# Performance work log

Hardware: AMD Instinct MI355X
Metric: run time of the kernel (lower is better)

Reference implementation:

```python
import jax, jax.numpy as jnp
import numpy as np

H, HKV, DH = 32, 8, 128
ROPE_BASE = 500000.0


def _rope(x, pos):
    # x: [B, H, T, D]; MLX non-traditional rope (split halves)
    D = x.shape[-1]
    half = D // 2
    freqs = ROPE_BASE ** (-(jnp.arange(half, dtype=jnp.float32) * 2.0 / D))  # [half]
    t = pos + jnp.arange(x.shape[2], dtype=jnp.float32)                      # [T]
    ang = t[:, None] * freqs[None, :]                                        # [T, half]
    cos, sin = jnp.cos(ang), jnp.sin(ang)
    x1, x2 = x[..., :half], x[..., half:]
    return jnp.concatenate([x1 * cos - x2 * sin, x1 * sin + x2 * cos], axis=-1)


def setup_inputs() -> dict:
    key = jax.random.key(0)
    ks = jax.random.split(key, 5)
    B, T, HID = 1, 2048, 4096
    s = 0.02
    return {
        "hidden_states": jax.random.normal(ks[0], (B, T, HID), jnp.float32),
        "Wq": jax.random.normal(ks[1], (H * DH, HID), jnp.float32) * s,
        "Wk": jax.random.normal(ks[2], (HKV * DH, HID), jnp.float32) * s,
        "Wv": jax.random.normal(ks[3], (HKV * DH, HID), jnp.float32) * s,
        "Wo": jax.random.normal(ks[4], (HID, H * DH), jnp.float32) * s,
        "k_cache": jnp.zeros((1, HKV, 4096, DH), jnp.float32),
        "v_cache": jnp.zeros((1, HKV, 4096, DH), jnp.float32),
        "pos_int": 0,
    }


def reference(hidden_states, Wq, Wk, Wv, Wo, k_cache, v_cache, pos_int):
    B, T, _ = hidden_states.shape
    # QKV projections (no bias, Llama-style) -> [B, h, T, D]
    q = (hidden_states @ Wq.T).reshape(B, T, H, DH).transpose(0, 2, 1, 3)
    k = (hidden_states @ Wk.T).reshape(B, T, HKV, DH).transpose(0, 2, 1, 3)
    v = (hidden_states @ Wv.T).reshape(B, T, HKV, DH).transpose(0, 2, 1, 3)
    # RoPE with position offset
    q = _rope(q, pos_int)
    k = _rope(k, pos_int)
    # KV-cache scatter update at pos_int, then window to [:pos_int+T]
    k_cache = jax.lax.dynamic_update_slice(k_cache, k, (0, 0, pos_int, 0))
    v_cache = jax.lax.dynamic_update_slice(v_cache, v, (0, 0, pos_int, 0))
    Tk = pos_int + T
    k_win = k_cache[:, :, :Tk, :]
    v_win = v_cache[:, :, :Tk, :]
    # GQA: repeat_interleave KV heads to match query heads
    group = H // HKV
    k_ = jnp.repeat(k_win, group, axis=1)   # [B, H, Tk, D]
    v_ = jnp.repeat(v_win, group, axis=1)
    # SDPA, is_causal=True => top-left aligned causal mask (query i sees keys j<=i)
    scale = 1.0 / jnp.sqrt(jnp.asarray(DH, jnp.float32))
    scores = jnp.einsum("bhtd,bhsd->bhts", q, k_) * scale  # [B, H, T, Tk]
    causal = jnp.arange(Tk)[None, :] <= jnp.arange(T)[:, None]
    scores = jnp.where(causal[None, None], scores, jnp.finfo(scores.dtype).min)
    attn = jax.nn.softmax(scores, axis=-1)
    out = jnp.einsum("bhts,bhsd->bhtd", attn, v_)           # [B, H, T, D]
    out = out.transpose(0, 2, 1, 3).reshape(B, T, H * DH)
    return out @ Wo.T
```

## Files before the change

kernel.cpp:

```cpp
#include <hip/hip_runtime.h>


#define DEVI __device__ __forceinline__

typedef __attribute__((ext_vector_type(8))) short short8;
typedef __attribute__((ext_vector_type(4))) float f32x4;

DEVI unsigned short f2bf(float f) {
  union { float f; unsigned u; } x; x.f = f;
  unsigned r = x.u + 0x7FFFu + ((x.u >> 16) & 1u);
  return (unsigned short)(r >> 16);
}
DEVI float bf2f(unsigned short h) {
  union { unsigned u; float f; } x; x.u = ((unsigned)h) << 16;
  return x.f;
}
DEVI f32x4 mfma16(short8 a, short8 b, f32x4 c) {
  return __builtin_amdgcn_mfma_f32_16x16x32_bf16(a, b, c, 0, 0, 0);
}
DEVI void gl2lds16(const unsigned short* g, unsigned short* l) {
  __builtin_amdgcn_global_load_lds(
      (const __attribute__((address_space(1))) unsigned int*)g,
      (__attribute__((address_space(3))) unsigned int*)l, 16, 0, 0);
}

__global__ __launch_bounds__(256)
void cvt_kernel(const float* __restrict__ src, unsigned short* __restrict__ dst,
                int n4) {
  int i = blockIdx.x * 256 + threadIdx.x;
  const int stride = gridDim.x * 256;
  for (; i < n4; i += stride) {
    float4 v = ((const float4*)src)[i];
    ushort4 h;
    h.x = f2bf(v.x); h.y = f2bf(v.y); h.z = f2bf(v.z); h.w = f2bf(v.w);
    ((ushort4*)dst)[i] = h;
  }
}

__global__ __launch_bounds__(256, 2)
void gemm_qkv_bf16(const unsigned short* __restrict__ hsb,
                   const unsigned short* __restrict__ Wqb,
                   const unsigned short* __restrict__ Wkb,
                   const unsigned short* __restrict__ Wvb,
                   unsigned short* __restrict__ Qb,
                   unsigned short* __restrict__ Kb,
                   unsigned short* __restrict__ Vb) {
  const int K = 4096;
  __shared__ __align__(16) unsigned short As[128][64];
  __shared__ __align__(16) unsigned short Bs[128][64];
  const int tid = threadIdx.x, lane = tid & 63, wid = tid >> 6;
  const int m0 = blockIdx.y * 128;
  const int n0g = blockIdx.x * 128;

  const unsigned short* Bsrc; unsigned short* outp; int ldo, oc;
  if (n0g < 4096)      { Bsrc = Wqb + (size_t)n0g * K;          outp = Qb; ldo = 4096; oc = n0g; }
  else if (n0g < 5120) { Bsrc = Wkb + (size_t)(n0g - 4096) * K; outp = Kb; ldo = 1024; oc = n0g - 4096; }
  else                 { Bsrc = Wvb + (size_t)(n0g - 5120) * K; outp = Vb; ldo = 1024; oc = n0g - 5120; }
  const unsigned short* Asrc = hsb + (size_t)m0 * K;

  f32x4 acc[4][4];
#pragma unroll
  for (int i = 0; i < 4; ++i)
#pragma unroll
    for (int j = 0; j < 4; ++j) acc[i][j] = (f32x4){0.f, 0.f, 0.f, 0.f};

  const int wm = (wid >> 1) * 64, wn = (wid & 1) * 64;
  const int srow = wid * 32 + (lane >> 3);
  const int scol = (lane & 7) * 8;

  for (int k0 = 0; k0 < K; k0 += 64) {
#pragma unroll
    for (int i = 0; i < 4; ++i) {
      gl2lds16(Asrc + (size_t)(srow + i * 8) * K + k0 + scol, &As[wid * 32 + i * 8][0]);
      gl2lds16(Bsrc + (size_t)(srow + i * 8) * K + k0 + scol, &Bs[wid * 32 + i * 8][0]);
    }
    __syncthreads();
#pragma unroll
    for (int ks = 0; ks < 2; ++ks) {
      short8 af[4], bfr[4];
      const int co = ks * 64 + ((lane >> 4) << 4);
#pragma unroll
      for (int i = 0; i < 4; ++i) {
        af[i]  = *(const short8*)((const char*)(&As[wm + i * 16 + (lane & 15)][0]) + co);
        bfr[i] = *(const short8*)((const char*)(&Bs[wn + i * 16 + (lane & 15)][0]) + co);
      }
#pragma unroll
      for (int i = 0; i < 4; ++i)
#pragma unroll
        for (int j = 0; j < 4; ++j)
          acc[i][j] = mfma16(af[i], bfr[j], acc[i][j]);
    }
    __syncthreads();
  }

#pragma unroll
  for (int i = 0; i < 4; ++i) {
    int rb = m0 + wm + i * 16 + ((lane >> 4) << 2);
#pragma unroll
    for (int j = 0; j < 4; ++j) {
      int cb = oc + wn + j * 16 + (lane & 15);
#pragma unroll
      for (int r = 0; r < 4; ++r)
        outp[(size_t)(rb + r) * ldo + cb] = f2bf(acc[i][j][r]);
    }
  }
}

__global__ __launch_bounds__(256)
void transpose_v(const unsigned short* __restrict__ Vb,
                 unsigned short* __restrict__ VtG) {
  __shared__ unsigned short tile[64][68];
  const int tid = threadIdx.x;
  const int t0 = blockIdx.x * 64;
  const int c0 = blockIdx.y * 64;
  const int r = tid >> 4;
  const int c4 = (tid & 15) << 2;
#pragma unroll
  for (int i = 0; i < 4; ++i) {
    ushort4 v = *(const ushort4*)(Vb + (size_t)(t0 + r + i * 16) * 1024 + c0 + c4);
    *(ushort4*)&tile[r + i * 16][c4] = v;
  }
  __syncthreads();
#pragma unroll
  for (int i = 0; i < 4; ++i) {
    int d = r + i * 16;
    ushort4 o;
    o.x = tile[c4 + 0][d]; o.y = tile[c4 + 1][d];
    o.z = tile[c4 + 2][d]; o.w = tile[c4 + 3][d];
    *(ushort4*)(VtG + (size_t)(c0 + d) * 2048 + t0 + c4) = o;
  }
}

__global__ __launch_bounds__(256)
void rope_kernel(unsigned short* __restrict__ Qb, unsigned short* __restrict__ Kb,
                 const int* __restrict__ posp) {
  const int QP = 2048 * 32 * 64;
  const int KP = 2048 * 8 * 64;
  int idx = blockIdx.x * 256 + threadIdx.x;
  if (idx >= QP + KP) return;
  unsigned short* base; int t, hh, d, ld;
  if (idx < QP) {
    base = Qb; ld = 4096;
    t = idx >> 11; int rem = idx & 2047; hh = rem >> 6; d = rem & 63;
  } else {
    int j = idx - QP; base = Kb; ld = 1024;
    t = j >> 9; int rem = j & 511; hh = rem >> 6; d = rem & 63;
  }
  float freq = exp2f(-(float)d * 0.29580575880077f);
  float ang = (float)(t + posp[0]) * freq;
  float s, c;
  __sincosf(ang, &s, &c);
  size_t i1 = (size_t)t * ld + hh * 128 + d;
  float x1 = bf2f(base[i1]), x2 = bf2f(base[i1 + 64]);
  base[i1]      = f2bf(x1 * c - x2 * s);
  base[i1 + 64] = f2bf(x1 * s + x2 * c);
}

__global__ __launch_bounds__(512, 4)
void attn_kernel(const unsigned short* __restrict__ Qb,
                 const unsigned short* __restrict__ Kb,
                 const unsigned short* __restrict__ VtG,
                 unsigned short* __restrict__ Ob) {
  __shared__ __align__(16) unsigned short Ks[64][128];
  __shared__ __align__(16) unsigned short Vt[128][64];
  __shared__ __align__(16) unsigned short Ps[8][16][64];
  const int tid = threadIdx.x, lane = tid & 63, w = tid >> 6;
  const int h = blockIdx.y;
  const int qt = (blockIdx.y >> 4) ? (15 - blockIdx.x) : blockIdx.x;
  const int kh = h >> 2;
  const int q0 = qt * 128;
  const float SCALE = 0.08838834764831845f;

  short8 aq[4];
  {
    const int qrow = q0 + w * 16 + (lane & 15);
#pragma unroll
    for (int ks = 0; ks < 4; ++ks)
      aq[ks] = *(const short8*)(Qb + (size_t)qrow * 4096 + h * 128 + ks * 32 +
                                ((lane >> 4) << 3));
  }

  f32x4 o_acc[8];
#pragma unroll
  for (int n8 = 0; n8 < 8; ++n8) o_acc[n8] = (f32x4){0.f, 0.f, 0.f, 0.f};
  float mst[4], lst[4];
#pragma unroll
  for (int r = 0; r < 4; ++r) { mst[r] = -1e30f; lst[r] = 0.f; }

  const int ksrow0 = w * 8 + (lane >> 4);
  const int vdrow0 = w * 16 + (lane >> 3);

  const int ntiles = 2 * (qt + 1);
  for (int st = 0; st < ntiles; ++st) {
    const int s0 = st * 64;
#pragma unroll
    for (int j = 0; j < 2; ++j) {
      int sr = ksrow0 + j * 4;
      int sc = (((lane & 15) << 4) ^ ((sr & 7) << 4)) >> 1;
      gl2lds16(Kb + (size_t)(s0 + sr) * 1024 + kh * 128 + sc, &Ks[w * 8 + j * 4][0]);
    }
#pragma unroll
    for (int j = 0; j < 2; ++j) {
      int dr = vdrow0 + j * 8;
      int sc = (((lane & 7) << 4) ^ ((dr & 7) << 4)) >> 1;
      gl2lds16(VtG + (size_t)(kh * 128 + dr) * 2048 + s0 + sc, &Vt[w * 16 + j * 8][0]);
    }
    __syncthreads();

    f32x4 sacc[4];
#pragma unroll
    for (int ni = 0; ni < 4; ++ni) sacc[ni] = (f32x4){0.f, 0.f, 0.f, 0.f};
#pragma unroll
    for (int ks = 0; ks < 4; ++ks) {
      const int co = ks * 64 + ((lane >> 4) << 4);
      short8 bk[4];
#pragma unroll
      for (int ni = 0; ni < 4; ++ni) {
        int kr = ni * 16 + (lane & 15);
        bk[ni] = *(const short8*)((const char*)(&Ks[kr][0]) + (co ^ ((kr & 7) << 4)));
      }
#pragma unroll
      for (int ni = 0; ni < 4; ++ni)
        sacc[ni] = mfma16(aq[ks], bk[ni], sacc[ni]);
    }

    char* pb = (char*)(&Ps[w][0][0]);
#pragma unroll
    for (int r = 0; r < 4; ++r) {
      const int qrow = q0 + w * 16 + ((lane >> 4) << 2) + r;
      float v4[4]; float vmax = -1e30f;
#pragma unroll
      for (int ni = 0; ni < 4; ++ni) {
        int scol = s0 + ni * 16 + (lane & 15);
        float x = sacc[ni][r] * SCALE;
        if (scol > qrow) x = -1e30f;
        v4[ni] = x; vmax = fmaxf(vmax, x);
      }
      vmax = fmaxf(vmax, __shfl_xor(vmax, 1));
      vmax = fmaxf(vmax, __shfl_xor(vmax, 2));
      vmax = fmaxf(vmax, __shfl_xor(vmax, 4));
      vmax = fmaxf(vmax, __shfl_xor(vmax, 8));
      float mo = mst[r];
      float mn = fmaxf(mo, vmax);
      float al = __expf(mo - mn);
      float rs = 0.f;
      const int prow = ((lane >> 4) << 2) + r;
      const int pswz = ((prow >> 2) & 3) << 5;
#pragma unroll
      for (int ni = 0; ni < 4; ++ni) {
        float p = __expf(v4[ni] - mn);
        rs += p;
        int cbyte = (ni * 16 + (lane & 15)) * 2;
        *(unsigned short*)(pb + prow * 128 + (cbyte ^ pswz)) = f2bf(p);
      }
      rs += __shfl_xor(rs, 1);
      rs += __shfl_xor(rs, 2);
      rs += __shfl_xor(rs, 4);
      rs += __shfl_xor(rs, 8);
      lst[r] = lst[r] * al + rs;
      mst[r] = mn;
#pragma unroll
      for (int n8 = 0; n8 < 8; ++n8) o_acc[n8][r] *= al;
    }

#pragma unroll
    for (int ks2 = 0; ks2 < 2; ++ks2) {
      const int co = ks2 * 64 + ((lane >> 4) << 4);
      const int pr = lane & 15;
      short8 pa = *(const short8*)(pb + pr * 128 + (co ^ (((pr >> 2) & 3) << 5)));
#pragma unroll
      for (int n8 = 0; n8 < 8; ++n8) {
        int vr = n8 * 16 + (lane & 15);
        short8 bv = *(const short8*)((const char*)(&Vt[vr][0]) + (co ^ ((vr & 7) << 4)));
        o_acc[n8] = mfma16(pa, bv, o_acc[n8]);
      }
    }
    __syncthreads();
  }

#pragma unroll
  for (int r = 0; r < 4; ++r) {
    float inv = 1.0f / lst[r];
    int row = q0 + w * 16 + ((lane >> 4) << 2) + r;
#pragma unroll
    for (int n8 = 0; n8 < 8; ++n8)
      Ob[(size_t)row * 4096 + h * 128 + n8 * 16 + (lane & 15)] =
          f2bf(o_acc[n8][r] * inv);
  }
}

__global__ __launch_bounds__(256, 2)
void gemm_out_bf16(const unsigned short* __restrict__ Ab,
                   const unsigned short* __restrict__ Wob,
                   float* __restrict__ Cout) {
  const int K = 4096;
  __shared__ __align__(16) unsigned short As[128][64];
  __shared__ __align__(16) unsigned short Bs[128][64];
  const int tid = threadIdx.x, lane = tid & 63, wid = tid >> 6;
  const int m0 = blockIdx.y * 128;
  const int n0 = blockIdx.x * 128;
  const unsigned short* Asrc = Ab + (size_t)m0 * K;
  const unsigned short* Bsrc = Wob + (size_t)n0 * K;

  f32x4 acc[4][4];
#pragma unroll
  for (int i = 0; i < 4; ++i)
#pragma unroll
    for (int j = 0; j < 4; ++j) acc[i][j] = (f32x4){0.f, 0.f, 0.f, 0.f};

  const int wm = (wid >> 1) * 64, wn = (wid & 1) * 64;
  const int srow = wid * 32 + (lane >> 3);
  const int scol = (lane & 7) * 8;

  for (int k0 = 0; k0 < K; k0 += 64) {
#pragma unroll
    for (int i = 0; i < 4; ++i) {
      gl2lds16(Asrc + (size_t)(srow + i * 8) * K + k0 + scol, &As[wid * 32 + i * 8][0]);
      gl2lds16(Bsrc + (size_t)(srow + i * 8) * K + k0 + scol, &Bs[wid * 32 + i * 8][0]);
    }
    __syncthreads();
#pragma unroll
    for (int ks = 0; ks < 2; ++ks) {
      short8 af[4], bfr[4];
      const int co = ks * 64 + ((lane >> 4) << 4);
#pragma unroll
      for (int i = 0; i < 4; ++i) {
        af[i]  = *(const short8*)((const char*)(&As[wm + i * 16 + (lane & 15)][0]) + co);
        bfr[i] = *(const short8*)((const char*)(&Bs[wn + i * 16 + (lane & 15)][0]) + co);
      }
#pragma unroll
      for (int i = 0; i < 4; ++i)
#pragma unroll
        for (int j = 0; j < 4; ++j)
          acc[i][j] = mfma16(af[i], bfr[j], acc[i][j]);
    }
    __syncthreads();
  }

#pragma unroll
  for (int i = 0; i < 4; ++i) {
    int rb = m0 + wm + i * 16 + ((lane >> 4) << 2);
#pragma unroll
    for (int j = 0; j < 4; ++j) {
      int cb = n0 + wn + j * 16 + (lane & 15);
#pragma unroll
      for (int r = 0; r < 4; ++r)
        Cout[(size_t)(rb + r) * 4096 + cb] = acc[i][j][r];
    }
  }
}

extern "C" void kernel_launch(void* const* d_in, const int* in_sizes, int n_in,
                              void* d_out, int out_size, void* d_ws, size_t ws_size,
                              hipStream_t stream) {
  const float* hs = (const float*)d_in[0];
  const float* Wq = (const float*)d_in[1];
  const float* Wk = (const float*)d_in[2];
  const float* Wv = (const float*)d_in[3];
  const float* Wo = (const float*)d_in[4];
  const int* pos = (const int*)d_in[7];

  unsigned short* hsb = (unsigned short*)d_ws;
  unsigned short* Wqb = hsb + (size_t)8  * 1024 * 1024;
  unsigned short* Wkb = Wqb + (size_t)16 * 1024 * 1024;
  unsigned short* Wvb = Wkb + (size_t)4  * 1024 * 1024;
  unsigned short* Wob = Wvb + (size_t)4  * 1024 * 1024;
  unsigned short* Qb  = Wob + (size_t)16 * 1024 * 1024;
  unsigned short* Kb  = Qb  + (size_t)8  * 1024 * 1024;
  unsigned short* Vb  = Kb  + (size_t)2  * 1024 * 1024;
  unsigned short* Ob  = Vb  + (size_t)2  * 1024 * 1024;
  unsigned short* VtG = hsb;
  float* out = (float*)d_out;

  cvt_kernel<<<dim3(2048), 256, 0, stream>>>(hs, hsb, 2 * 1024 * 1024);
  cvt_kernel<<<dim3(2048), 256, 0, stream>>>(Wq, Wqb, 4 * 1024 * 1024);
  cvt_kernel<<<dim3(1024), 256, 0, stream>>>(Wk, Wkb, 1 * 1024 * 1024);
  cvt_kernel<<<dim3(1024), 256, 0, stream>>>(Wv, Wvb, 1 * 1024 * 1024);
  cvt_kernel<<<dim3(2048), 256, 0, stream>>>(Wo, Wob, 4 * 1024 * 1024);

  gemm_qkv_bf16<<<dim3(48, 16), 256, 0, stream>>>(hsb, Wqb, Wkb, Wvb, Qb, Kb, Vb);
  transpose_v<<<dim3(32, 16), 256, 0, stream>>>(Vb, VtG);
  const int npairs = 2048 * 32 * 64 + 2048 * 8 * 64;
  rope_kernel<<<dim3((npairs + 255) / 256), 256, 0, stream>>>(Qb, Kb, pos);
  attn_kernel<<<dim3(16, 32), 512, 0, stream>>>(Qb, Kb, VtG, Ob);
  gemm_out_bf16<<<dim3(32, 16), 256, 0, stream>>>(Ob, Wob, out);
}
```

Measured before the change: 380.5 us.

## Rewrite QKV GEMM as 256x256 double-buffered 8-wave pipelined kernel

Replaces the 128x128 single-buffered QKV projection GEMM with a 256x256 tile, 512-thread kernel. It double-buffers LDS, uses an XOR swizzle to avoid bank conflicts, and splits each K-step into four phases that interleave global-to-LDS prefetch with MFMA bursts under s_setprio. This is meant to hide load latency and raise arithmetic intensity per block. The grid shrinks to 192 blocks, which may underfill the 256 CUs, and the hand-tuned waitcnt and barrier schedule is fragile.

```diff
diff --git a/kernel.cpp b/kernel.cpp
--- a/kernel.cpp
+++ b/kernel.cpp
@@ -23,6 +23,8 @@
       (const __attribute__((address_space(1))) unsigned int*)g,
       (__attribute__((address_space(3))) unsigned int*)l, 16, 0, 0);
 }
+DEVI void bar() { __builtin_amdgcn_s_barrier(); }
+DEVI void sfence() { __builtin_amdgcn_sched_barrier(0); }
 
 __global__ __launch_bounds__(256)
 void cvt_kernel(const float* __restrict__ src, unsigned short* __restrict__ dst,
@@ -37,20 +39,21 @@
   }
 }
 
-__global__ __launch_bounds__(256, 2)
-void gemm_qkv_bf16(const unsigned short* __restrict__ hsb,
-                   const unsigned short* __restrict__ Wqb,
-                   const unsigned short* __restrict__ Wkb,
-                   const unsigned short* __restrict__ Wvb,
-                   unsigned short* __restrict__ Qb,
-                   unsigned short* __restrict__ Kb,
-                   unsigned short* __restrict__ Vb) {
+__global__ __launch_bounds__(512, 2)
+void gemm_qkv_8ph(const unsigned short* __restrict__ hsb,
+                  const unsigned short* __restrict__ Wqb,
+                  const unsigned short* __restrict__ Wkb,
+                  const unsigned short* __restrict__ Wvb,
+                  unsigned short* __restrict__ Qb,
+                  unsigned short* __restrict__ Kb,
+                  unsigned short* __restrict__ Vb) {
   const int K = 4096;
-  __shared__ __align__(16) unsigned short As[128][64];
-  __shared__ __align__(16) unsigned short Bs[128][64];
-  const int tid = threadIdx.x, lane = tid & 63, wid = tid >> 6;
-  const int m0 = blockIdx.y * 128;
-  const int n0g = blockIdx.x * 128;
+  const int NT = 64;
+  __shared__ __align__(16) unsigned short Ls[2][2][2][256][32];
+  const int tid = threadIdx.x, lane = tid & 63, w = tid >> 6;
+  const int wr = w >> 2, wc = w & 3;
+  const int m0 = blockIdx.y * 256;
+  const int n0g = blockIdx.x * 256;
 
   const unsigned short* Bsrc; unsigned short* outp; int ldo, oc;
   if (n0g < 4096)      { Bsrc = Wqb + (size_t)n0g * K;          outp = Qb; ldo = 4096; oc = n0g; }
@@ -58,50 +61,108 @@
   else                 { Bsrc = Wvb + (size_t)(n0g - 5120) * K; outp = Vb; ldo = 1024; oc = n0g - 5120; }
   const unsigned short* Asrc = hsb + (size_t)m0 * K;
 
-  f32x4 acc[4][4];
-#pragma unroll
-  for (int i = 0; i < 4; ++i)
+  auto stageU = [&](const unsigned short* src, int ab, int kh, int tt, int bb) {
+#pragma unroll
+    for (int j = 0; j < 2; ++j) {
+      const int seg = j * 8 + w;
+      const int row = seg * 16 + (lane >> 2);
+      const int cs  = (lane & 3) ^ ((row >> 1) & 3);
+      gl2lds16(src + (size_t)row * K + tt * 64 + kh * 32 + cs * 8,
+               &Ls[bb][ab][kh][seg * 16][0]);
+    }
+  };
+  auto ldA = [&](int bb, int kh, int fm) -> short8 {
+    const int ra = wr * 128 + fm * 16 + (lane & 15);
+    const int cs = (lane >> 4) ^ ((ra >> 1) & 3);
+    return *(const short8*)&Ls[bb][0][kh][ra][cs * 8];
+  };
+  auto ldB = [&](int bb, int kh, int fn) -> short8 {
+    const int rb = wc * 64 + fn * 16 + (lane & 15);
+    const int cs = (lane >> 4) ^ ((rb >> 1) & 3);
+    return *(const short8*)&Ls[bb][1][kh][rb][cs * 8];
+  };
+
+  f32x4 acc[8][4];
+#pragma unroll
+  for (int i = 0; i < 8; ++i)
 #pragma unroll
     for (int j = 0; j < 4; ++j) acc[i][j] = (f32x4){0.f, 0.f, 0.f, 0.f};
 
-  const int wm = (wid >> 1) * 64, wn = (wid & 1) * 64;
-  const int srow = wid * 32 + (lane >> 3);
-  const int scol = (lane & 7) * 8;
-
-  for (int k0 = 0; k0 < K; k0 += 64) {
-#pragma unroll
-    for (int i = 0; i < 4; ++i) {
-      gl2lds16(Asrc + (size_t)(srow + i * 8) * K + k0 + scol, &As[wid * 32 + i * 8][0]);
-      gl2lds16(Bsrc + (size_t)(srow + i * 8) * K + k0 + scol, &Bs[wid * 32 + i * 8][0]);
-    }
-    __syncthreads();
-#pragma unroll
-    for (int ks = 0; ks < 2; ++ks) {
-      short8 af[4], bfr[4];
-      const int co = ks * 64 + ((lane >> 4) << 4);
-#pragma unroll
-      for (int i = 0; i < 4; ++i) {
-        af[i]  = *(const short8*)((const char*)(&As[wm + i * 16 + (lane & 15)][0]) + co);
-        bfr[i] = *(const short8*)((const char*)(&Bs[wn + i * 16 + (lane & 15)][0]) + co);
-      }
-#pragma unroll
-      for (int i = 0; i < 4; ++i)
-#pragma unroll
-        for (int j = 0; j < 4; ++j)
-          acc[i][j] = mfma16(af[i], bfr[j], acc[i][j]);
-    }
-    __syncthreads();
-  }
-
-#pragma unroll
-  for (int i = 0; i < 4; ++i) {
-    int rb = m0 + wm + i * 16 + ((lane >> 4) << 2);
-#pragma unroll
-    for (int j = 0; j < 4; ++j) {
-      int cb = oc + wn + j * 16 + (lane & 15);
+  stageU(Asrc, 0, 0, 0, 0);
+  stageU(Asrc, 0, 1, 0, 0);
+  stageU(Bsrc, 1, 0, 0, 0);
+  stageU(Bsrc, 1, 1, 0, 0);
+  stageU(Bsrc, 1, 0, 1, 1);
+  stageU(Asrc, 0, 0, 1, 1);
+  stageU(Bsrc, 1, 1, 1, 1);
+  asm volatile("s_waitcnt vmcnt(6)" ::: "memory");
+  bar();
+  sfence();
+
+  short8 af[4], bfr[4];
+  for (int t = 0; t < NT; ++t) {
+    const int bb = t & 1, nb = bb ^ 1;
+#pragma unroll
+    for (int i = 0; i < 4; ++i) af[i] = ldA(bb, 0, i);
+#pragma unroll
+    for (int i = 0; i < 4; ++i) bfr[i] = ldB(bb, 0, i);
+    if (t + 1 < NT) stageU(Asrc, 0, 1, t + 1, nb);
+    bar();
+    __builtin_amdgcn_s_setprio(1);
+#pragma unroll
+    for (int i = 0; i < 4; ++i)
+#pragma unroll
+      for (int j = 0; j < 4; ++j) acc[i][j] = mfma16(af[i], bfr[j], acc[i][j]);
+    __builtin_amdgcn_s_setprio(0);
+    sfence(); bar(); sfence();
+#pragma unroll
+    for (int i = 0; i < 4; ++i) af[i] = ldA(bb, 0, 4 + i);
+    if (t + 2 < NT) stageU(Bsrc, 1, 0, t + 2, bb);
+    bar();
+    __builtin_amdgcn_s_setprio(1);
+#pragma unroll
+    for (int i = 0; i < 4; ++i)
+#pragma unroll
+      for (int j = 0; j < 4; ++j) acc[4 + i][j] = mfma16(af[i], bfr[j], acc[4 + i][j]);
+    __builtin_amdgcn_s_setprio(0);
+    sfence(); bar(); sfence();
+#pragma unroll
+    for (int i = 0; i < 4; ++i) af[i] = ldA(bb, 1, i);
+#pragma unroll
+    for (int i = 0; i < 4; ++i) bfr[i] = ldB(bb, 1, i);
+    if (t + 2 < NT) stageU(Asrc, 0, 0, t + 2, bb);
+    bar();
+    __builtin_amdgcn_s_setprio(1);
+#pragma unroll
+    for (int i = 0; i < 4; ++i)
+#pragma unroll
+      for (int j = 0; j < 4; ++j) acc[i][j] = mfma16(af[i], bfr[j], acc[i][j]);
+    __builtin_amdgcn_s_setprio(0);
+    sfence(); bar(); sfence();
+#pragma unroll
+    for (int i = 0; i < 4; ++i) af[i] = ldA(bb, 1, 4 + i);
+    if (t + 2 < NT) stageU(Bsrc, 1, 1, t + 2, bb);
+    bar();
+    __builtin_amdgcn_s_setprio(1);
+#pragma unroll
+    for (int i = 0; i < 4; ++i)
+#pragma unroll
+      for (int j = 0; j < 4; ++j) acc[4 + i][j] = mfma16(af[i], bfr[j], acc[4 + i][j]);
+    __builtin_amdgcn_s_setprio(0);
+    if (t < NT - 2) asm volatile("s_waitcnt vmcnt(6)" ::: "memory");
+    else            asm volatile("s_waitcnt vmcnt(0)" ::: "memory");
+    sfence(); bar(); sfence();
+  }
+
+#pragma unroll
+  for (int fm = 0; fm < 8; ++fm) {
+    const int rb0 = m0 + wr * 128 + fm * 16 + ((lane >> 4) << 2);
+#pragma unroll
+    for (int fn = 0; fn < 4; ++fn) {
+      const int cb = oc + wc * 64 + fn * 16 + (lane & 15);
 #pragma unroll
       for (int r = 0; r < 4; ++r)
-        outp[(size_t)(rb + r) * ldo + cb] = f2bf(acc[i][j][r]);
+        outp[(size_t)(rb0 + r) * ldo + cb] = f2bf(acc[fm][fn][r]);
     }
   }
 }
@@ -378,7 +439,7 @@
   cvt_kernel<<<dim3(1024), 256, 0, stream>>>(Wv, Wvb, 1 * 1024 * 1024);
   cvt_kernel<<<dim3(2048), 256, 0, stream>>>(Wo, Wob, 4 * 1024 * 1024);
 
-  gemm_qkv_bf16<<<dim3(48, 16), 256, 0, stream>>>(hsb, Wqb, Wkb, Wvb, Qb, Kb, Vb);
+  gemm_qkv_8ph<<<dim3(24, 8), 512, 0, stream>>>(hsb, Wqb, Wkb, Wvb, Qb, Kb, Vb);
   transpose_v<<<dim3(32, 16), 256, 0, stream>>>(Vb, VtG);
   const int npairs = 2048 * 32 * 64 + 2048 * 8 * 64;
   rope_kernel<<<dim3((npairs + 255) / 256), 256, 0, stream>>>(Qb, Kb, pos);
```

Result: faster. 367.4 us (-3.4%).
